# Optimization experiments

Hardware: AMD Instinct MI355X
Metric: run time of the kernel (lower is better)

Reference implementation:

```python
import jax, jax.numpy as jnp
import numpy as np

POSE_NUM = 8192
EDGE_NUM = 1048576  # n*p = 8192*128
E = EDGE_NUM        # number of gathered edges


def setup_inputs() -> dict:
    key = jax.random.key(0)
    k1, k2, k3, k4, k5, k6 = jax.random.split(key, 6)
    # poses: [1, POSE_NUM, 7] = (tx,ty,tz, qx,qy,qz,qw) with unit quaternion (pypose SE3 convention)
    t = jax.random.normal(k1, (1, POSE_NUM, 3), jnp.float32) * 5.0
    q = jax.random.normal(k2, (1, POSE_NUM, 4), jnp.float32)
    q = q / jnp.linalg.norm(q, axis=-1, keepdims=True)
    poses = jnp.concatenate([t, q], axis=-1)
    # patch coords (r, theta): r in [1, 51], theta in [-pi, pi]
    u = jax.random.uniform(k3, (1, EDGE_NUM, 2), jnp.float32)
    r = 1.0 + 50.0 * u[..., 0:1]
    theta = (2.0 * u[..., 1:2] - 1.0) * jnp.float32(np.pi)
    patch_coords = jnp.concatenate([r, theta], axis=-1)
    # elevation angle phi: small angles typical of sonar beams
    elevation_angle = jax.random.normal(k4, (1, EDGE_NUM, 1), jnp.float32) * 0.3
    # target coords (in init_ba these come from a transform + delta; random is math-equivalent for the residual)
    target_coords = jax.random.normal(k5, (1, E, 2), jnp.float32)
    poses_idx = jax.random.randint(k6, (E,), 0, POSE_NUM, jnp.int32)
    patch_idx = jax.random.randint(jax.random.fold_in(k6, 1), (E,), 0, EDGE_NUM, jnp.int32)
    return {"poses": poses, "patch_coords": patch_coords, "elevation_angle": elevation_angle,
            "target_coords": target_coords, "poses_idx": poses_idx, "patch_idx": patch_idx}


def reference(poses, patch_coords, elevation_angle, target_coords, poses_idx, patch_idx):
    # --- gather per-edge data ---
    p = poses[0, poses_idx]                    # [E, 7]
    rt = patch_coords[0, patch_idx]            # [E, 2] (r, theta)
    phi = elevation_angle[0, patch_idx, 0]     # [E]
    r, theta = rt[:, 0], rt[:, 1]
    # --- polar -> cartesian (spherical sonar convention) ---
    cphi = jnp.cos(phi)
    pts = jnp.stack([r * cphi * jnp.cos(theta),
                     r * cphi * jnp.sin(theta),
                     r * jnp.sin(phi)], axis=-1)        # [E, 3]
    # --- SE3 action: R(q) @ pts + t, q = (qx,qy,qz,qw) unit quaternion ---
    t, qv, qw = p[:, :3], p[:, 3:6], p[:, 6:7]
    uv = jnp.cross(qv, pts)
    pts_w = pts + 2.0 * (qw * uv + jnp.cross(qv, uv)) + t  # [E, 3]
    # --- cartesian -> polar; residual only needs (r, theta) ---
    x, y, z = pts_w[:, 0], pts_w[:, 1], pts_w[:, 2]
    r_out = jnp.sqrt(x * x + y * y + z * z)
    theta_out = jnp.arctan2(y, x)
    proj = jnp.stack([r_out, theta_out], axis=-1)[None]   # [1, E, 2]
    return proj - target_coords
```

## Files before the change

kernel.cpp:

```cpp
#include <hip/hip_runtime.h>
#include <math.h>


#define POSE_NUM 8192

__global__ __launch_bounds__(256) void repack_poses_kernel(
    const float* __restrict__ poses,
    float4* __restrict__ pose8)
{
    int i = blockIdx.x * blockDim.x + threadIdx.x;
    if (i >= POSE_NUM) return;
    const float* p = poses + i * 7;
    pose8[i * 2 + 0] = make_float4(p[0], p[1], p[2], p[3]);
    pose8[i * 2 + 1] = make_float4(p[4], p[5], p[6], 0.0f);
}

__device__ __forceinline__ float fast_atan2f(float y, float x) {
    float ax = fabsf(x), ay = fabsf(y);
    float mx = fmaxf(ax, ay), mn = fminf(ax, ay);
    float t = mn * __builtin_amdgcn_rcpf(fmaxf(mx, 1e-30f));
    float s = t * t;
    float r = fmaf(s, fmaf(s, fmaf(s, fmaf(s, 0.0208351f, -0.0851330f),
                                   0.1801410f), -0.3302995f), 0.9998660f) * t;
    if (ay > ax) r = 1.5707963267948966f - r;
    if (x < 0.0f) r = 3.14159265358979f - r;
    return y < 0.0f ? -r : r;
}

__device__ __forceinline__ void edge_compute(
    int pi, int ki,
    const float2* __restrict__ patch_coords,
    const float*  __restrict__ elev,
    const float4* __restrict__ pose8,
    float tgx, float tgy, float* ox, float* oy)
{
    const float2 rt  = patch_coords[ki];
    const float  phi = elev[ki];
    const float  r = rt.x, theta = rt.y;

    float sphi, cphi, st, ct;
    __sincosf(phi,   &sphi, &cphi);
    __sincosf(theta, &st,   &ct);

    const float rc = r * cphi;
    const float px = rc * ct;
    const float py = rc * st;
    const float pz = r * sphi;

    const float4 pa = pose8[pi * 2 + 0];
    const float4 pb = pose8[pi * 2 + 1];
    const float tx = pa.x, ty = pa.y, tz = pa.z;
    const float qx = pa.w, qy = pb.x, qz = pb.y, qw = pb.z;

    const float ux = qy * pz - qz * py;
    const float uy = qz * px - qx * pz;
    const float uz = qx * py - qy * px;
    const float cx = qy * uz - qz * uy;
    const float cy = qz * ux - qx * uz;
    const float cz = qx * uy - qy * ux;

    const float x = px + 2.0f * (qw * ux + cx) + tx;
    const float y = py + 2.0f * (qw * uy + cy) + ty;
    const float z = pz + 2.0f * (qw * uz + cz) + tz;

    *ox = sqrtf(x * x + y * y + z * z) - tgx;
    *oy = fast_atan2f(y, x) - tgy;
}

__global__ __launch_bounds__(256) void ba_edge_kernel2(
    const float2* __restrict__ patch_coords,
    const float*  __restrict__ elev,
    const float2* __restrict__ target,
    const int*    __restrict__ poses_idx,
    const int*    __restrict__ patch_idx,
    const float4* __restrict__ pose8,
    float4*       __restrict__ out,
    int half_n)
{
    int t = blockIdx.x * blockDim.x + threadIdx.x;
    if (t >= half_n) return;

    const int2 pidx = ((const int2*)poses_idx)[t];
    const int2 kidx = ((const int2*)patch_idx)[t];
    const float4 tg = ((const float4*)target)[t];

    float4 o;
    edge_compute(pidx.x, kidx.x, patch_coords, elev, pose8, tg.x, tg.y, &o.x, &o.y);
    edge_compute(pidx.y, kidx.y, patch_coords, elev, pose8, tg.z, tg.w, &o.z, &o.w);
    out[t] = o;
}

__global__ __launch_bounds__(256) void ba_edge_kernel1(
    const float*  __restrict__ poses,
    const float2* __restrict__ patch_coords,
    const float*  __restrict__ elev,
    const float2* __restrict__ target,
    const int*    __restrict__ poses_idx,
    const int*    __restrict__ patch_idx,
    float2*       __restrict__ out,
    int n)
{
    int e = blockIdx.x * blockDim.x + threadIdx.x;
    if (e >= n) return;
    const int pi = poses_idx[e];
    const int ki = patch_idx[e];
    const float2 rt  = patch_coords[ki];
    const float  phi = elev[ki];
    float sphi, cphi, st, ct;
    __sincosf(phi, &sphi, &cphi);
    __sincosf(rt.y, &st, &ct);
    const float rc = rt.x * cphi;
    const float px = rc * ct, py = rc * st, pz = rt.x * sphi;
    const float* p = poses + pi * 7;
    const float tx = p[0], ty = p[1], tz = p[2];
    const float qx = p[3], qy = p[4], qz = p[5], qw = p[6];
    const float ux = qy * pz - qz * py;
    const float uy = qz * px - qx * pz;
    const float uz = qx * py - qy * px;
    const float cx = qy * uz - qz * uy;
    const float cy = qz * ux - qx * uz;
    const float cz = qx * uy - qy * ux;
    const float x = px + 2.0f * (qw * ux + cx) + tx;
    const float y = py + 2.0f * (qw * uy + cy) + ty;
    const float z = pz + 2.0f * (qw * uz + cz) + tz;
    const float2 tg = target[e];
    out[e] = make_float2(sqrtf(x * x + y * y + z * z) - tg.x,
                         fast_atan2f(y, x) - tg.y);
}

extern "C" void kernel_launch(void* const* d_in, const int* in_sizes, int n_in,
                              void* d_out, int out_size, void* d_ws, size_t ws_size,
                              hipStream_t stream) {
    const float*  poses        = (const float*)d_in[0];
    const float2* patch_coords = (const float2*)d_in[1];
    const float*  elev         = (const float*)d_in[2];
    const float2* target       = (const float2*)d_in[3];
    const int*    poses_idx    = (const int*)d_in[4];
    const int*    patch_idx    = (const int*)d_in[5];
    const int n = in_sizes[4];

    const size_t pose8_bytes = (size_t)POSE_NUM * 8 * sizeof(float);

    if (ws_size >= pose8_bytes && (n & 1) == 0) {
        float4* pose8 = (float4*)d_ws;
        repack_poses_kernel<<<(POSE_NUM + 255) / 256, 256, 0, stream>>>(poses, pose8);
        const int half_n = n / 2;
        ba_edge_kernel2<<<(half_n + 255) / 256, 256, 0, stream>>>(
            patch_coords, elev, target, poses_idx, patch_idx, pose8,
            (float4*)d_out, half_n);
    } else {
        ba_edge_kernel1<<<(n + 255) / 256, 256, 0, stream>>>(
            poses, patch_coords, elev, target, poses_idx, patch_idx,
            (float2*)d_out, n);
    }
}
```

Measured before the change: 41.37 us.

## Precompute per-patch Cartesian points into workspace before edge gather

A new precompute kernel converts every patch's (r, theta, phi) into a Cartesian float4 in workspace, and also repacks the poses. The edge kernel then gathers one 16-byte point per edge instead of two separate gathers from patch_coords and elevation, and does no trig. The aim is fewer random gather transactions and less per-edge math. In exchange there is an extra full pass over all patches, with about 12MB read and 16MB written. Since edges and patches are equal in number, the trig work is not reduced overall.

```diff
diff --git a/kernel.cpp b/kernel.cpp
--- a/kernel.cpp
+++ b/kernel.cpp
@@ -2,18 +2,9 @@
 #include <math.h>
 
 
-#define POSE_NUM 8192
-
-__global__ __launch_bounds__(256) void repack_poses_kernel(
-    const float* __restrict__ poses,
-    float4* __restrict__ pose8)
-{
-    int i = blockIdx.x * blockDim.x + threadIdx.x;
-    if (i >= POSE_NUM) return;
-    const float* p = poses + i * 7;
-    pose8[i * 2 + 0] = make_float4(p[0], p[1], p[2], p[3]);
-    pose8[i * 2 + 1] = make_float4(p[4], p[5], p[6], 0.0f);
-}
+#define POSE_NUM   8192
+#define PTS_BYTES  (16u * 1024u * 1024u)
+#define POSE8_OFF  PTS_BYTES
 
 __device__ __forceinline__ float fast_atan2f(float y, float x) {
     float ax = fabsf(x), ay = fabsf(y);
@@ -27,28 +18,36 @@
     return y < 0.0f ? -r : r;
 }
 
-__device__ __forceinline__ void edge_compute(
-    int pi, int ki,
+__global__ __launch_bounds__(256) void precompute_kernel(
     const float2* __restrict__ patch_coords,
     const float*  __restrict__ elev,
-    const float4* __restrict__ pose8,
+    const float*  __restrict__ poses,
+    float4* __restrict__ pts,
+    float4* __restrict__ pose8,
+    int npatch)
+{
+    int i = blockIdx.x * blockDim.x + threadIdx.x;
+    if (i < npatch) {
+        const float2 rt = patch_coords[i];
+        const float phi = elev[i];
+        float sphi, cphi, st, ct;
+        __sincosf(phi,  &sphi, &cphi);
+        __sincosf(rt.y, &st,   &ct);
+        const float rc = rt.x * cphi;
+        pts[i] = make_float4(rc * ct, rc * st, rt.x * sphi, 0.0f);
+    }
+    if (i < POSE_NUM) {
+        const float* p = poses + i * 7;
+        pose8[i * 2 + 0] = make_float4(p[0], p[1], p[2], p[3]);
+        pose8[i * 2 + 1] = make_float4(p[4], p[5], p[6], 0.0f);
+    }
+}
+
+__device__ __forceinline__ void edge_finish(
+    float4 P, float4 pa, float4 pb,
     float tgx, float tgy, float* ox, float* oy)
 {
-    const float2 rt  = patch_coords[ki];
-    const float  phi = elev[ki];
-    const float  r = rt.x, theta = rt.y;
-
-    float sphi, cphi, st, ct;
-    __sincosf(phi,   &sphi, &cphi);
-    __sincosf(theta, &st,   &ct);
-
-    const float rc = r * cphi;
-    const float px = rc * ct;
-    const float py = rc * st;
-    const float pz = r * sphi;
-
-    const float4 pa = pose8[pi * 2 + 0];
-    const float4 pb = pose8[pi * 2 + 1];
+    const float px = P.x, py = P.y, pz = P.z;
     const float tx = pa.x, ty = pa.y, tz = pa.z;
     const float qx = pa.w, qy = pb.x, qz = pb.y, qw = pb.z;
 
@@ -67,13 +66,12 @@
     *oy = fast_atan2f(y, x) - tgy;
 }
 
-__global__ __launch_bounds__(256) void ba_edge_kernel2(
-    const float2* __restrict__ patch_coords,
-    const float*  __restrict__ elev,
+__global__ __launch_bounds__(256) void edge_kernel(
+    const float4* __restrict__ pts,
+    const float4* __restrict__ pose8,
     const float2* __restrict__ target,
     const int*    __restrict__ poses_idx,
     const int*    __restrict__ patch_idx,
-    const float4* __restrict__ pose8,
     float4*       __restrict__ out,
     int half_n)
 {
@@ -84,9 +82,16 @@
     const int2 kidx = ((const int2*)patch_idx)[t];
     const float4 tg = ((const float4*)target)[t];
 
+    const float4 P0 = pts[kidx.x];
+    const float4 P1 = pts[kidx.y];
+    const float4 a0 = pose8[2 * pidx.x + 0];
+    const float4 b0 = pose8[2 * pidx.x + 1];
+    const float4 a1 = pose8[2 * pidx.y + 0];
+    const float4 b1 = pose8[2 * pidx.y + 1];
+
     float4 o;
-    edge_compute(pidx.x, kidx.x, patch_coords, elev, pose8, tg.x, tg.y, &o.x, &o.y);
-    edge_compute(pidx.y, kidx.y, patch_coords, elev, pose8, tg.z, tg.w, &o.z, &o.w);
+    edge_finish(P0, a0, b0, tg.x, tg.y, &o.x, &o.y);
+    edge_finish(P1, a1, b1, tg.z, tg.w, &o.z, &o.w);
     out[t] = o;
 }
 
@@ -137,17 +142,21 @@
     const float2* target       = (const float2*)d_in[3];
     const int*    poses_idx    = (const int*)d_in[4];
     const int*    patch_idx    = (const int*)d_in[5];
-    const int n = in_sizes[4];
 
-    const size_t pose8_bytes = (size_t)POSE_NUM * 8 * sizeof(float);
+    const int n      = in_sizes[4];
+    const int npatch = in_sizes[2];
 
-    if (ws_size >= pose8_bytes && (n & 1) == 0) {
-        float4* pose8 = (float4*)d_ws;
-        repack_poses_kernel<<<(POSE_NUM + 255) / 256, 256, 0, stream>>>(poses, pose8);
+    const size_t need = (size_t)npatch * 16 + (size_t)POSE_NUM * 32;
+
+    if (ws_size >= need && (n & 1) == 0 && npatch * 16u <= PTS_BYTES) {
+        float4* pts   = (float4*)d_ws;
+        float4* pose8 = (float4*)((char*)d_ws + POSE8_OFF);
+        const int pre_grid = (npatch + 255) / 256;
+        precompute_kernel<<<pre_grid, 256, 0, stream>>>(
+            patch_coords, elev, poses, pts, pose8, npatch);
         const int half_n = n / 2;
-        ba_edge_kernel2<<<(half_n + 255) / 256, 256, 0, stream>>>(
-            patch_coords, elev, target, poses_idx, patch_idx, pose8,
-            (float4*)d_out, half_n);
+        edge_kernel<<<(half_n + 255) / 256, 256, 0, stream>>>(
+            pts, pose8, target, poses_idx, patch_idx, (float4*)d_out, half_n);
     } else {
         ba_edge_kernel1<<<(n + 255) / 256, 256, 0, stream>>>(
             poses, patch_coords, elev, target, poses_idx, patch_idx,
```

Measured after the change: 37.07 us. 10.4% less time.
